# Kernel tuning notes

Hardware: AMD Instinct MI355X
Metric: run time of the kernel (lower is better)

Reference implementation:

```python
import jax, jax.numpy as jnp
import numpy as np

N_NODES = 5000
N_EDGES = 160000


def _conv2d(x, w, b):
    # x: [N, Cin, H, W], w: [Cout, Cin, kh, kw] (OIHW), VALID padding, stride 1
    out = jax.lax.conv_general_dilated(
        x, w, window_strides=(1, 1), padding='VALID',
        dimension_numbers=('NCHW', 'OIHW', 'NCHW'))
    return out + b[None, :, None, None]


def _gcn_norm(edge_index, n):
    # PyG gcn_norm with add_self_loops=False: deg from target (col) nodes,
    # norm = d^{-1/2}[src] * d^{-1/2}[dst]
    src, dst = edge_index[0], edge_index[1]
    ones = jnp.ones((edge_index.shape[1],), jnp.float32)
    deg = jax.ops.segment_sum(ones, dst, num_segments=n)
    dinv = jnp.where(deg > 0, jax.lax.rsqrt(jnp.maximum(deg, 1.0)), 0.0)
    return dinv[src] * dinv[dst]


def _arma(x, edge_index, norm, w_init, w_root, bias):
    # ARMAConv, num_layers=1: mean_k ReLU( Ahat (x W_k) + x V_k + b_k )
    # x: [N, Fin], w_init/w_root: [K, Fin, Fout], bias: [K, Fout]
    n = x.shape[0]
    src, dst = edge_index[0], edge_index[1]
    h = jnp.einsum('nf,kfo->kno', x, w_init)            # [K, N, Fout]
    msg = h[:, src, :] * norm[None, :, None]            # [K, E, Fout] gather
    agg = jax.vmap(lambda m: jax.ops.segment_sum(m, dst, num_segments=n))(msg)
    root = jnp.einsum('nf,kfo->kno', x, w_root)         # [K, N, Fout]
    out = jax.nn.relu(agg + root + bias[:, None, :])
    return out.mean(axis=0)                             # mean over K stacks


def setup_inputs() -> dict:
    key = jax.random.key(0)
    ks = jax.random.split(key, 32)

    def rn(i, shape, s=0.1):
        return jax.random.normal(ks[i], shape, jnp.float32) * s

    d = {}
    d['inputs'] = jax.random.normal(ks[0], (N_NODES, 1, 53, 6), jnp.float32)
    d['edge_index'] = jax.random.randint(ks[1], (2, N_EDGES), 0, N_NODES, jnp.int32)
    # CNN encoder params (Conv2d(1,100,(3,3)), Conv2d(100,200,(3,2)), Conv2d(200,1,(3,2)))
    d['e1_w'] = rn(2, (100, 1, 3, 3), 0.3); d['e1_b'] = rn(3, (100,), 0.1)
    d['e2_w'] = rn(4, (200, 100, 3, 2), 0.04); d['e2_b'] = rn(5, (200,), 0.1)
    d['e3_w'] = rn(6, (1, 200, 3, 2), 0.04); d['e3_b'] = rn(7, (1,), 0.1)
    # ARMA layers: (Fin, Fout, num_stacks K)
    dims = [(94, 128, 2), (128, 128, 2), (128, 128, 2), (128, 128, 2), (128, 128, 2), (128, 16, 1)]
    k = 8
    for i, (fi, fo, K) in enumerate(dims, 1):
        s = 1.0 / np.sqrt(fi)
        d[f'a{i}_wi'] = rn(k, (K, fi, fo), s)
        d[f'a{i}_wr'] = rn(k + 1, (K, fi, fo), s)
        d[f'a{i}_b'] = rn(k + 2, (K, fo), 0.05)
        k += 3
    return d


def reference(inputs, edge_index, e1_w, e1_b, e2_w, e2_b, e3_w, e3_b,
              a1_wi, a1_wr, a1_b, a2_wi, a2_wr, a2_b, a3_wi, a3_wr, a3_b,
              a4_wi, a4_wr, a4_b, a5_wi, a5_wr, a5_b, a6_wi, a6_wr, a6_b):
    # CNN encoder (Dropout2d is identity in eval mode)
    h = jax.nn.leaky_relu(_conv2d(inputs, e1_w, e1_b), 0.01)
    h = jax.nn.leaky_relu(_conv2d(h, e2_w, e2_b), 0.01)
    h = _conv2d(h, e3_w, e3_b)
    h = jnp.tanh(h.reshape(-1, 94))                     # [N, 94]
    norm = _gcn_norm(edge_index, h.shape[0])
    for (wi, wr, b) in [(a1_wi, a1_wr, a1_b), (a2_wi, a2_wr, a2_b),
                        (a3_wi, a3_wr, a3_b), (a4_wi, a4_wr, a4_b),
                        (a5_wi, a5_wr, a5_b)]:
        h = jnp.tanh(_arma(h, edge_index, norm, wi, wr, b))
    h = _arma(h, edge_index, norm, a6_wi, a6_wr, a6_b)
    return jax.nn.softmax(h, axis=1)
```

## Files before the change

### kernel.cpp

```cpp
#include <hip/hip_runtime.h>
#include <math.h>

typedef _Float16 f16;
typedef _Float16 f16x4 __attribute__((ext_vector_type(4)));
typedef _Float16 f16x8 __attribute__((ext_vector_type(8)));
typedef float f32x4 __attribute__((ext_vector_type(4)));

#define NN 5000
#define NE 160000

#define OFF_W2T   0ul
#define OFF_W3T   344064ul
#define OFF_WT1   346560ul
#define OFF_WT2   444864ul
#define OFF_WT3   575936ul
#define OFF_WT4   707008ul
#define OFF_WT5   838080ul
#define OFF_WT6   969152ul
#define OFF_H0    985536ul
#define OFF_HA    1945536ul
#define OFF_HB    3225536ul
#define OFF_C     4505536ul
#define OFF_DEG   14745536ul
#define OFF_IP    14765536ul
#define OFF_CUR   14785568ul
#define OFF_DINV  14805568ul
#define OFF_CSRS  14825568ul
#define OFF_CSRN  15465568ul
#define OFF_W1T   OFF_C

#define L_IN   0
#define L_BUF  1280
#define L_A1   (L_BUF)
#define L_C1   (L_BUF + 16640)
#define L_C2   (L_BUF)
#define C1_STRIDE 136
#define LDS_TOTAL (17920 + 208*272)

__global__ void prep_w2t(const float* __restrict__ w, f16* __restrict__ W2T) {
  int i = blockIdx.x*256 + threadIdx.x;
  if (i >= 21*256*32) return;
  int j = i & 7, g = (i >> 3) & 3, n = (i >> 5) & 255, kc = i >> 13;
  int k = kc*32 + g*8 + j;
  int tap = k / 112, c = k - tap*112;
  float v = 0.f;
  if (n < 200 && c < 100 && tap < 6) v = w[n*600 + c*6 + tap];
  W2T[i] = (f16)v;
}

__global__ void prep_w3t(const float* __restrict__ w, f16* __restrict__ W3T) {
  int i = blockIdx.x*256 + threadIdx.x;
  if (i >= 1248) return;
  int tap = i / 208, c = i - tap*208;
  float v = (c < 200) ? w[c*6 + tap] : 0.f;
  W3T[i] = (f16)v;
}

__global__ void prep_w1t(const float* __restrict__ w, f16* __restrict__ W1T) {
  int i = blockIdx.x*256 + threadIdx.x;
  if (i >= 112*32) return;
  int n = i >> 5, k = i & 31;
  float v = (n < 100 && k < 9) ? w[n*9 + k] : 0.f;
  W1T[i] = (f16)v;
}

__global__ void prep_wt(const float* __restrict__ wi, const float* __restrict__ wr,
                        f16* __restrict__ WT, int Kst, int Fin, int Fout, int Kpad, int R) {
  int i = blockIdx.x*256 + threadIdx.x;
  if (i >= R*Kpad) return;
  int n = i / Kpad, kk = i - n*Kpad;
  float v = 0.f;
  if (kk < Fin) {
    int path = n / (Kst*Fout);
    if (path < 2) {
      int rem = n - path*(Kst*Fout);
      int k = rem / Fout, fo = rem - k*Fout;
      const float* w = (path == 0) ? wi : wr;
      v = w[(k*Fin + kk)*Fout + fo];
    }
  }
  WT[i] = (f16)v;
}

__global__ void zero_kernel(int* __restrict__ deg, int* __restrict__ cur) {
  int i = blockIdx.x*256 + threadIdx.x;
  if (i < NN) { deg[i] = 0; cur[i] = 0; }
}

__global__ void deg_kernel(const int* __restrict__ ei, int* __restrict__ deg) {
  int e = blockIdx.x*256 + threadIdx.x;
  if (e < NE) atomicAdd(&deg[ei[NE + e]], 1);
}

__global__ __launch_bounds__(1024) void scan_kernel(const int* __restrict__ deg,
                                                    int* __restrict__ ip,
                                                    float* __restrict__ dinv) {
  __shared__ int buf[1024];
  __shared__ int s_carry;
  const int tid = threadIdx.x;
  if (tid == 0) s_carry = 0;
  __syncthreads();
  for (int base = 0; base < NN; base += 1024) {
    int i = base + tid;
    int v = (i < NN) ? deg[i] : 0;
    buf[tid] = v;
    __syncthreads();
    for (int off = 1; off < 1024; off <<= 1) {
      int t = (tid >= off) ? buf[tid - off] : 0;
      __syncthreads();
      buf[tid] += t;
      __syncthreads();
    }
    int incl = buf[tid];
    int c = s_carry;
    if (i < NN) {
      ip[i] = c + incl - v;
      dinv[i] = (v > 0) ? rsqrtf((float)v) : 0.f;
    }
    __syncthreads();
    if (tid == 1023) s_carry = c + buf[1023];
    __syncthreads();
  }
  if (tid == 0) ip[NN] = s_carry;
}

__global__ void csr_fill(const int* __restrict__ ei, const float* __restrict__ dinv,
                         const int* __restrict__ ip, int* __restrict__ cur,
                         int* __restrict__ csrs, float* __restrict__ csrn) {
  int e = blockIdx.x*256 + threadIdx.x;
  if (e >= NE) return;
  int s = ei[e], d = ei[NE + e];
  int pos = ip[d] + atomicAdd(&cur[d], 1);
  csrs[pos] = s;
  csrn[pos] = dinv[s]*dinv[d];
}

__global__ __launch_bounds__(1024) void cnn_kernel(
    const float* __restrict__ inp, const f16* __restrict__ W1T, const float* __restrict__ b1,
    const f16* __restrict__ W2T, const float* __restrict__ b2,
    const f16* __restrict__ W3T, const float* __restrict__ b3,
    f16* __restrict__ h0)
{
  extern __shared__ char smem[];
  float* s_in = (float*)(smem + L_IN);
  f16*   s_a1 = (f16*)(smem + L_A1);
  f16*   s_c1 = (f16*)(smem + L_C1);
  f16*   s_c2 = (f16*)(smem + L_C2);

  const int node = blockIdx.x;
  const int tid  = threadIdx.x;
  const int lane = tid & 63, wid = tid >> 6;
  const int l15 = lane & 15, g = lane >> 4;

  for (int i = tid; i < 318; i += 1024) s_in[i] = inp[node*318 + i];
  for (int i = tid; i < 208*12; i += 1024) {
    int r = i / 12, c = 100 + (i - r*12);
    s_c1[r*C1_STRIDE + c] = (f16)0.f;
  }
  __syncthreads();

  for (int i = tid; i < 208*32; i += 1024) {
    int m = i >> 5, k = i & 31;
    float v = 0.f;
    if (m < 204 && k < 9) {
      int y = m >> 2, x = m & 3;
      int ky = (k >= 6) ? 2 : (k >= 3 ? 1 : 0);
      int kx = k - ky*3;
      v = s_in[(y + ky)*6 + x + kx];
    }
    s_a1[m*40 + k] = (f16)v;
  }
  __syncthreads();

  for (int p = wid; p < 91; p += 16) {
    int mt = p % 13, nt = p / 13;
    f16x8 a = *(const f16x8*)(W1T + (nt*16 + l15)*32 + g*8);
    f16x8 b = *(const f16x8*)(s_a1 + (mt*16 + l15)*40 + g*8);
    f32x4 acc = (f32x4){0.f,0.f,0.f,0.f};
    acc = __builtin_amdgcn_mfma_f32_16x16x32_f16(a, b, acc, 0, 0, 0);
    int m = mt*16 + l15;
    int cb = nt*16 + g*4;
    f16x4 pack;
    #pragma unroll
    for (int j = 0; j < 4; j++) {
      int c = cb + j;
      float bias = (c < 100) ? b1[c] : 0.f;
      float v = acc[j] + bias;
      v = v > 0.f ? v : 0.01f*v;
      pack[j] = (f16)v;
    }
    *(f16x4*)(s_c1 + m*C1_STRIDE + cb) = pack;
  }
  __syncthreads();

  const int wm = wid >> 3, wn = wid & 7;

  const f16* abase[5];
  #pragma unroll
  for (int mi = 0; mi < 5; mi++) {
    int p = (wm*5 + mi)*16 + l15;
    int pp = p < 147 ? p : 0;
    int y2 = pp / 3;
    abase[mi] = s_c1 + (y2*4 + (pp - y2*3))*C1_STRIDE + g*8;
  }

  f32x4 acc[5][2];
  #pragma unroll
  for (int mi = 0; mi < 5; mi++)
    #pragma unroll
    for (int ni = 0; ni < 2; ni++)
      acc[mi][ni] = (f32x4){0.f,0.f,0.f,0.f};

  const f16* bbase = W2T + wn*1024 + l15*32 + g*8;
  #pragma unroll
  for (int kc = 0; kc < 21; kc++) {
    f16x8 b[2];
    const f16* bkc = bbase + kc*8192;
    #pragma unroll
    for (int ni = 0; ni < 2; ni++)
      b[ni] = *(const f16x8*)(bkc + ni*512);
    int kg0 = kc*32;
    int tap0 = kg0 / 112;
    int rem0 = kg0 - tap0*112;
    int cfull = rem0 + g*8;
    int wrap = cfull >= 112 ? 1 : 0;
    int c = cfull - wrap*112;
    int tapg = tap0 + wrap;
    int dr = ((tapg >> 1) << 2) + (tapg & 1);
    int aoff = dr*C1_STRIDE + (c - g*8);
    #pragma unroll
    for (int mi = 0; mi < 5; mi++) {
      f16x8 a = *(const f16x8*)(abase[mi] + aoff);
      #pragma unroll
      for (int ni = 0; ni < 2; ni++)
        acc[mi][ni] = __builtin_amdgcn_mfma_f32_16x16x32_f16(b[ni], a, acc[mi][ni], 0, 0, 0);
    }
  }

  __syncthreads();

  #pragma unroll
  for (int ni = 0; ni < 2; ni++) {
    int nb = wn*32 + ni*16 + g*4;
    if (nb < 216) {
      #pragma unroll
      for (int mi = 0; mi < 5; mi++) {
        int m = (wm*5 + mi)*16 + l15;
        if (m < 147) {
          f16x4 pack;
          #pragma unroll
          for (int j = 0; j < 4; j++) {
            int n = nb + j;
            float bias = (n < 200) ? b2[n] : 0.f;
            float v = acc[mi][ni][j] + bias;
            v = v > 0.f ? v : 0.01f*v;
            pack[j] = (f16)v;
          }
          *(f16x4*)(s_c2 + m*216 + nb) = pack;
        }
      }
    }
  }
  __syncthreads();

  if (wid < 6) {
    int pos = wid*16 + l15;
    int q = pos < 94 ? pos : 0;
    int r3 = (q >> 1)*3 + (q & 1);
    f32x4 acc3 = (f32x4){0.f,0.f,0.f,0.f};
    #pragma unroll
    for (int kc = 0; kc < 39; kc++) {
      int k = kc*32 + g*8;
      int tap = k / 208;
      int c = k - tap*208;
      int dr = (tap >> 1)*3 + (tap & 1);
      f16x8 a = *(const f16x8*)(W3T + k);
      f16x8 b = *(const f16x8*)(s_c2 + (r3 + dr)*216 + c);
      acc3 = __builtin_amdgcn_mfma_f32_16x16x32_f16(a, b, acc3, 0, 0, 0);
    }
    if (g == 0) {
      float v = (pos < 94) ? tanhf(acc3[0] + b3[0]) : 0.f;
      h0[node*96 + pos] = (f16)v;
    }
  }
}

template<int K>
__global__ __launch_bounds__(256, 4) void gemm_kernel(
    const f16* __restrict__ A, const f16* __restrict__ B, float* __restrict__ C,
    int M, int N)
{
  constexpr int LK = K + 8;
  __shared__ f16 sA[64*LK];
  __shared__ f16 sB[64*LK];
  const int tid = threadIdx.x;
  const int m0 = blockIdx.x*64, n0 = blockIdx.y*64;
  constexpr int SEGS = K/8;
  for (int i = tid; i < 64*SEGS; i += 256) {
    int row = i / SEGS, seg = i - row*SEGS;
    int gm = m0 + row; if (gm >= M) gm = M - 1;
    *(f16x8*)(sA + row*LK + seg*8) = *(const f16x8*)(A + (size_t)gm*K + seg*8);
    *(f16x8*)(sB + row*LK + seg*8) = *(const f16x8*)(B + (size_t)(n0 + row)*K + seg*8);
  }
  __syncthreads();
  const int lane = tid & 63, wid = tid >> 6;
  const int l15 = lane & 15, g = lane >> 4;
  const int wm = wid >> 1, wn = wid & 1;
  f32x4 acc[2][2];
  #pragma unroll
  for (int mi = 0; mi < 2; mi++)
    #pragma unroll
    for (int ni = 0; ni < 2; ni++)
      acc[mi][ni] = (f32x4){0.f,0.f,0.f,0.f};
  #pragma unroll
  for (int kc = 0; kc < K/32; kc++) {
    f16x8 a[2], b[2];
    #pragma unroll
    for (int mi = 0; mi < 2; mi++)
      a[mi] = *(const f16x8*)(sA + (wm*32 + mi*16 + l15)*LK + kc*32 + g*8);
    #pragma unroll
    for (int ni = 0; ni < 2; ni++)
      b[ni] = *(const f16x8*)(sB + (wn*32 + ni*16 + l15)*LK + kc*32 + g*8);
    #pragma unroll
    for (int mi = 0; mi < 2; mi++)
      #pragma unroll
      for (int ni = 0; ni < 2; ni++)
        acc[mi][ni] = __builtin_amdgcn_mfma_f32_16x16x32_f16(a[mi], b[ni], acc[mi][ni], 0, 0, 0);
  }
  #pragma unroll
  for (int mi = 0; mi < 2; mi++)
    #pragma unroll
    for (int ni = 0; ni < 2; ni++)
      #pragma unroll
      for (int j = 0; j < 4; j++) {
        int m = m0 + wm*32 + mi*16 + g*4 + j;
        int n = n0 + wn*32 + ni*16 + l15;
        if (m < M) C[(size_t)m*N + n] = acc[mi][ni][j];
      }
}

__global__ __launch_bounds__(256) void combine128(
    const float* __restrict__ C, const int* __restrict__ ip,
    const int* __restrict__ csrs, const float* __restrict__ csrn,
    const float* __restrict__ bias, f16* __restrict__ hout)
{
  const int d = blockIdx.x*4 + (threadIdx.x >> 6);
  const int lane = threadIdx.x & 63;
  const int i0 = ip[d], i1 = ip[d+1];
  float a00 = 0.f, a01 = 0.f, a10 = 0.f, a11 = 0.f;
  float b00 = 0.f, b01 = 0.f, b10 = 0.f, b11 = 0.f;
  int e = i0;
  for (; e + 1 < i1; e += 2) {
    int s0 = csrs[e], s1 = csrs[e+1];
    float w0 = csrn[e], w1 = csrn[e+1];
    const float* t0 = C + (size_t)s0*512;
    const float* t1 = C + (size_t)s1*512;
    a00 += w0*t0[lane];       a01 += w0*t0[lane+64];
    a10 += w0*t0[lane+128];   a11 += w0*t0[lane+192];
    b00 += w1*t1[lane];       b01 += w1*t1[lane+64];
    b10 += w1*t1[lane+128];   b11 += w1*t1[lane+192];
  }
  if (e < i1) {
    int s = csrs[e];
    float w = csrn[e];
    const float* t = C + (size_t)s*512;
    a00 += w*t[lane];       a01 += w*t[lane+64];
    a10 += w*t[lane+128];   a11 += w*t[lane+192];
  }
  a00 += b00; a01 += b01; a10 += b10; a11 += b11;
  const float* r = C + (size_t)d*512 + 256;
  float o0 = fmaxf(a00 + r[lane]     + bias[lane],     0.f)
           + fmaxf(a10 + r[lane+128] + bias[lane+128], 0.f);
  float o1 = fmaxf(a01 + r[lane+64]  + bias[lane+64],  0.f)
           + fmaxf(a11 + r[lane+192] + bias[lane+192], 0.f);
  hout[(size_t)d*128 + lane]      = (f16)tanhf(0.5f*o0);
  hout[(size_t)d*128 + lane + 64] = (f16)tanhf(0.5f*o1);
}

__global__ __launch_bounds__(256) void combine_out(
    const float* __restrict__ C, const int* __restrict__ ip,
    const int* __restrict__ csrs, const float* __restrict__ csrn,
    const float* __restrict__ bias, float* __restrict__ out)
{
  const int d = blockIdx.x*4 + (threadIdx.x >> 6);
  const int lane = threadIdx.x & 63;
  const int f = lane & 15;
  const int i0 = ip[d], i1 = ip[d+1];
  float a = 0.f, b = 0.f;
  int e = i0;
  for (; e + 1 < i1; e += 2) {
    a += csrn[e]   * C[(size_t)csrs[e]*64 + f];
    b += csrn[e+1] * C[(size_t)csrs[e+1]*64 + f];
  }
  if (e < i1) a += csrn[e] * C[(size_t)csrs[e]*64 + f];
  a += b;
  float v = fmaxf(a + C[(size_t)d*64 + 16 + f] + bias[f], 0.f);
  float m = v;
  #pragma unroll
  for (int off = 1; off < 16; off <<= 1) m = fmaxf(m, __shfl_xor(m, off));
  float ev = expf(v - m);
  float s = ev;
  #pragma unroll
  for (int off = 1; off < 16; off <<= 1) s += __shfl_xor(s, off);
  if (lane < 16) out[(size_t)d*16 + lane] = ev / s;
}

extern "C" void kernel_launch(void* const* d_in, const int* in_sizes, int n_in,
                              void* d_out, int out_size, void* d_ws, size_t ws_size,
                              hipStream_t stream)
{
  const float* inputs = (const float*)d_in[0];
  const int*   ei     = (const int*)d_in[1];
  const float* e1w = (const float*)d_in[2];
  const float* e1b = (const float*)d_in[3];
  const float* e2w = (const float*)d_in[4];
  const float* e2b = (const float*)d_in[5];
  const float* e3w = (const float*)d_in[6];
  const float* e3b = (const float*)d_in[7];
  const float *awi[6], *awr[6], *ab[6];
  for (int i = 0; i < 6; i++) {
    awi[i] = (const float*)d_in[8 + 3*i];
    awr[i] = (const float*)d_in[9 + 3*i];
    ab[i]  = (const float*)d_in[10 + 3*i];
  }
  char* ws = (char*)d_ws;
  f16* W2T = (f16*)(ws + OFF_W2T);
  f16* W3T = (f16*)(ws + OFF_W3T);
  f16* W1T = (f16*)(ws + OFF_W1T);
  f16* WT[6] = { (f16*)(ws + OFF_WT1), (f16*)(ws + OFF_WT2), (f16*)(ws + OFF_WT3),
                 (f16*)(ws + OFF_WT4), (f16*)(ws + OFF_WT5), (f16*)(ws + OFF_WT6) };
  f16* H0 = (f16*)(ws + OFF_H0);
  f16* HA = (f16*)(ws + OFF_HA);
  f16* HB = (f16*)(ws + OFF_HB);
  float* C = (float*)(ws + OFF_C);
  int* DEG = (int*)(ws + OFF_DEG);
  int* IP  = (int*)(ws + OFF_IP);
  int* CUR = (int*)(ws + OFF_CUR);
  float* DINV = (float*)(ws + OFF_DINV);
  int* CSRS = (int*)(ws + OFF_CSRS);
  float* CSRN = (float*)(ws + OFF_CSRN);

  (void)hipFuncSetAttribute((const void*)cnn_kernel,
                            hipFuncAttributeMaxDynamicSharedMemorySize, LDS_TOTAL);

  prep_w2t<<<672, 256, 0, stream>>>(e2w, W2T);
  prep_w3t<<<5, 256, 0, stream>>>(e3w, W3T);
  prep_w1t<<<14, 256, 0, stream>>>(e1w, W1T);
  prep_wt<<<192, 256, 0, stream>>>(awi[0], awr[0], WT[0], 2, 94, 128, 96, 512);
  for (int l = 1; l < 5; l++)
    prep_wt<<<256, 256, 0, stream>>>(awi[l], awr[l], WT[l], 2, 128, 128, 128, 512);
  prep_wt<<<32, 256, 0, stream>>>(awi[5], awr[5], WT[5], 1, 128, 16, 128, 64);

  zero_kernel<<<20, 256, 0, stream>>>(DEG, CUR);
  deg_kernel<<<625, 256, 0, stream>>>(ei, DEG);
  scan_kernel<<<1, 1024, 0, stream>>>(DEG, IP, DINV);
  csr_fill<<<625, 256, 0, stream>>>(ei, DINV, IP, CUR, CSRS, CSRN);

  cnn_kernel<<<NN, 1024, LDS_TOTAL, stream>>>(inputs, W1T, e1b, W2T, e2b, W3T, e3b, H0);

  gemm_kernel<96><<<dim3(79, 8), 256, 0, stream>>>(H0, WT[0], C, NN, 512);
  combine128<<<1250, 256, 0, stream>>>(C, IP, CSRS, CSRN, ab[0], HA);
  gemm_kernel<128><<<dim3(79, 8), 256, 0, stream>>>(HA, WT[1], C, NN, 512);
  combine128<<<1250, 256, 0, stream>>>(C, IP, CSRS, CSRN, ab[1], HB);
  gemm_kernel<128><<<dim3(79, 8), 256, 0, stream>>>(HB, WT[2], C, NN, 512);
  combine128<<<1250, 256, 0, stream>>>(C, IP, CSRS, CSRN, ab[2], HA);
  gemm_kernel<128><<<dim3(79, 8), 256, 0, stream>>>(HA, WT[3], C, NN, 512);
  combine128<<<1250, 256, 0, stream>>>(C, IP, CSRS, CSRN, ab[3], HB);
  gemm_kernel<128><<<dim3(79, 8), 256, 0, stream>>>(HB, WT[4], C, NN, 512);
  combine128<<<1250, 256, 0, stream>>>(C, IP, CSRS, CSRN, ab[4], HA);
  gemm_kernel<128><<<dim3(79, 1), 256, 0, stream>>>(HA, WT[5], C, NN, 64);
  combine_out<<<1250, 256, 0, stream>>>(C, IP, CSRS, CSRN, ab[5], (float*)d_out);
}
```

Before: 714.5 us.

## Store gathered GEMM output in fp16, fuse weight prep, reorder conv1 LDS rows

The layer GEMM now writes the Ahat-path half of its output as a separate fp16 buffer. The root half stays fp32 in its own array, so the edge gather in combine128 reads half as many bytes per neighbor, and each lane now handles an adjacent pair of columns. All weight-prep kernels are merged into one launch, and the zeroing kernel becomes hipMemsetAsync calls. The conv1 output rows in LDS are permuted by x-position (row = y + 52*x), and the zero-fill of padding columns 100..111 is dropped. Risks: fp16 rounding of aggregated messages, and the padding columns are no longer explicitly cleared, though they are multiplied by zero weights.

```diff
diff --git a/kernel.cpp b/kernel.cpp
--- a/kernel.cpp
+++ b/kernel.cpp
@@ -2,6 +2,7 @@
 #include <math.h>
 
 typedef _Float16 f16;
+typedef _Float16 f16x2 __attribute__((ext_vector_type(2)));
 typedef _Float16 f16x4 __attribute__((ext_vector_type(4)));
 typedef _Float16 f16x8 __attribute__((ext_vector_type(8)));
 typedef float f32x4 __attribute__((ext_vector_type(4)));
@@ -21,6 +22,7 @@
 #define OFF_HA    1945536ul
 #define OFF_HB    3225536ul
 #define OFF_C     4505536ul
+#define OFF_CT    9625536ul
 #define OFF_DEG   14745536ul
 #define OFF_IP    14765536ul
 #define OFF_CUR   14785568ul
@@ -37,37 +39,8 @@
 #define C1_STRIDE 136
 #define LDS_TOTAL (17920 + 208*272)
 
-__global__ void prep_w2t(const float* __restrict__ w, f16* __restrict__ W2T) {
-  int i = blockIdx.x*256 + threadIdx.x;
-  if (i >= 21*256*32) return;
-  int j = i & 7, g = (i >> 3) & 3, n = (i >> 5) & 255, kc = i >> 13;
-  int k = kc*32 + g*8 + j;
-  int tap = k / 112, c = k - tap*112;
-  float v = 0.f;
-  if (n < 200 && c < 100 && tap < 6) v = w[n*600 + c*6 + tap];
-  W2T[i] = (f16)v;
-}
-
-__global__ void prep_w3t(const float* __restrict__ w, f16* __restrict__ W3T) {
-  int i = blockIdx.x*256 + threadIdx.x;
-  if (i >= 1248) return;
-  int tap = i / 208, c = i - tap*208;
-  float v = (c < 200) ? w[c*6 + tap] : 0.f;
-  W3T[i] = (f16)v;
-}
-
-__global__ void prep_w1t(const float* __restrict__ w, f16* __restrict__ W1T) {
-  int i = blockIdx.x*256 + threadIdx.x;
-  if (i >= 112*32) return;
-  int n = i >> 5, k = i & 31;
-  float v = (n < 100 && k < 9) ? w[n*9 + k] : 0.f;
-  W1T[i] = (f16)v;
-}
-
-__global__ void prep_wt(const float* __restrict__ wi, const float* __restrict__ wr,
-                        f16* __restrict__ WT, int Kst, int Fin, int Fout, int Kpad, int R) {
-  int i = blockIdx.x*256 + threadIdx.x;
-  if (i >= R*Kpad) return;
+__device__ __forceinline__ void wt_body(int i, const float* wi, const float* wr,
+                                        f16* WT, int Kst, int Fin, int Fout, int Kpad) {
   int n = i / Kpad, kk = i - n*Kpad;
   float v = 0.f;
   if (kk < Fin) {
@@ -82,9 +55,48 @@
   WT[i] = (f16)v;
 }
 
-__global__ void zero_kernel(int* __restrict__ deg, int* __restrict__ cur) {
-  int i = blockIdx.x*256 + threadIdx.x;
-  if (i < NN) { deg[i] = 0; cur[i] = 0; }
+__global__ void prep_all(char* ws, const float* __restrict__ e1w,
+                         const float* __restrict__ e2w, const float* __restrict__ e3w,
+                         const float* wi1, const float* wr1, const float* wi2, const float* wr2,
+                         const float* wi3, const float* wr3, const float* wi4, const float* wr4,
+                         const float* wi5, const float* wr5, const float* wi6, const float* wr6) {
+  int b = blockIdx.x, tid = threadIdx.x;
+  if (b < 672) {
+    int i = b*256 + tid;
+    int kc = i >> 13, n = (i >> 5) & 255;
+    int k = i & 31;
+    int kk = kc*32 + k;
+    int tap = kk / 112, c = kk - tap*112;
+    float v = 0.f;
+    if (n < 200 && c < 100 && tap < 6) v = e2w[n*600 + c*6 + tap];
+    ((f16*)(ws + OFF_W2T))[i] = (f16)v;
+  } else if (b < 677) {
+    int i = (b - 672)*256 + tid;
+    if (i < 1248) {
+      int tap = i / 208, c = i - tap*208;
+      float v = (c < 200) ? e3w[c*6 + tap] : 0.f;
+      ((f16*)(ws + OFF_W3T))[i] = (f16)v;
+    }
+  } else if (b < 691) {
+    int i = (b - 677)*256 + tid;
+    if (i < 112*32) {
+      int n = i >> 5, k = i & 31;
+      float v = (n < 100 && k < 9) ? e1w[n*9 + k] : 0.f;
+      ((f16*)(ws + OFF_W1T))[i] = (f16)v;
+    }
+  } else if (b < 883) {
+    wt_body((b - 691)*256 + tid, wi1, wr1, (f16*)(ws + OFF_WT1), 2, 94, 128, 96);
+  } else if (b < 1139) {
+    wt_body((b - 883)*256 + tid, wi2, wr2, (f16*)(ws + OFF_WT2), 2, 128, 128, 128);
+  } else if (b < 1395) {
+    wt_body((b - 1139)*256 + tid, wi3, wr3, (f16*)(ws + OFF_WT3), 2, 128, 128, 128);
+  } else if (b < 1651) {
+    wt_body((b - 1395)*256 + tid, wi4, wr4, (f16*)(ws + OFF_WT4), 2, 128, 128, 128);
+  } else if (b < 1907) {
+    wt_body((b - 1651)*256 + tid, wi5, wr5, (f16*)(ws + OFF_WT5), 2, 128, 128, 128);
+  } else {
+    wt_body((b - 1907)*256 + tid, wi6, wr6, (f16*)(ws + OFF_WT6), 1, 128, 16, 128);
+  }
 }
 
 __global__ void deg_kernel(const int* __restrict__ ei, int* __restrict__ deg) {
@@ -153,10 +165,6 @@
   const int l15 = lane & 15, g = lane >> 4;
 
   for (int i = tid; i < 318; i += 1024) s_in[i] = inp[node*318 + i];
-  for (int i = tid; i < 208*12; i += 1024) {
-    int r = i / 12, c = 100 + (i - r*12);
-    s_c1[r*C1_STRIDE + c] = (f16)0.f;
-  }
   __syncthreads();
 
   for (int i = tid; i < 208*32; i += 1024) {
@@ -179,6 +187,7 @@
     f32x4 acc = (f32x4){0.f,0.f,0.f,0.f};
     acc = __builtin_amdgcn_mfma_f32_16x16x32_f16(a, b, acc, 0, 0, 0);
     int m = mt*16 + l15;
+    int rowp = (m >> 2) + 52*(m & 3);
     int cb = nt*16 + g*4;
     f16x4 pack;
     #pragma unroll
@@ -189,7 +198,7 @@
       v = v > 0.f ? v : 0.01f*v;
       pack[j] = (f16)v;
     }
-    *(f16x4*)(s_c1 + m*C1_STRIDE + cb) = pack;
+    *(f16x4*)(s_c1 + rowp*C1_STRIDE + cb) = pack;
   }
   __syncthreads();
 
@@ -201,7 +210,8 @@
     int p = (wm*5 + mi)*16 + l15;
     int pp = p < 147 ? p : 0;
     int y2 = pp / 3;
-    abase[mi] = s_c1 + (y2*4 + (pp - y2*3))*C1_STRIDE + g*8;
+    int x2 = pp - y2*3;
+    abase[mi] = s_c1 + (y2 + 52*x2)*C1_STRIDE + g*8;
   }
 
   f32x4 acc[5][2];
@@ -226,7 +236,7 @@
     int wrap = cfull >= 112 ? 1 : 0;
     int c = cfull - wrap*112;
     int tapg = tap0 + wrap;
-    int dr = ((tapg >> 1) << 2) + (tapg & 1);
+    int dr = (tapg >> 1) + 52*(tapg & 1);
     int aoff = dr*C1_STRIDE + (c - g*8);
     #pragma unroll
     for (int mi = 0; mi < 5; mi++) {
@@ -287,8 +297,8 @@
 
 template<int K>
 __global__ __launch_bounds__(256, 4) void gemm_kernel(
-    const f16* __restrict__ A, const f16* __restrict__ B, float* __restrict__ C,
-    int M, int N)
+    const f16* __restrict__ A, const f16* __restrict__ B, float* __restrict__ Croot,
+    f16* __restrict__ CT, int M, int N)
 {
   constexpr int LK = K + 8;
   __shared__ f16 sA[64*LK];
@@ -327,54 +337,83 @@
       for (int ni = 0; ni < 2; ni++)
         acc[mi][ni] = __builtin_amdgcn_mfma_f32_16x16x32_f16(a[mi], b[ni], acc[mi][ni], 0, 0, 0);
   }
-  #pragma unroll
-  for (int mi = 0; mi < 2; mi++)
-    #pragma unroll
-    for (int ni = 0; ni < 2; ni++)
+  if (CT != nullptr && n0 < 256) {
+    #pragma unroll
+    for (int mi = 0; mi < 2; mi++)
       #pragma unroll
-      for (int j = 0; j < 4; j++) {
-        int m = m0 + wm*32 + mi*16 + g*4 + j;
-        int n = n0 + wn*32 + ni*16 + l15;
-        if (m < M) C[(size_t)m*N + n] = acc[mi][ni][j];
-      }
+      for (int ni = 0; ni < 2; ni++)
+        #pragma unroll
+        for (int j = 0; j < 4; j++) {
+          int m = m0 + wm*32 + mi*16 + g*4 + j;
+          int n = n0 + wn*32 + ni*16 + l15;
+          if (m < M) CT[(size_t)m*256 + n] = (f16)acc[mi][ni][j];
+        }
+  } else if (CT != nullptr) {
+    #pragma unroll
+    for (int mi = 0; mi < 2; mi++)
+      #pragma unroll
+      for (int ni = 0; ni < 2; ni++)
+        #pragma unroll
+        for (int j = 0; j < 4; j++) {
+          int m = m0 + wm*32 + mi*16 + g*4 + j;
+          int n = n0 + wn*32 + ni*16 + l15 - 256;
+          if (m < M) Croot[(size_t)m*256 + n] = acc[mi][ni][j];
+        }
+  } else {
+    #pragma unroll
+    for (int mi = 0; mi < 2; mi++)
+      #pragma unroll
+      for (int ni = 0; ni < 2; ni++)
+        #pragma unroll
+        for (int j = 0; j < 4; j++) {
+          int m = m0 + wm*32 + mi*16 + g*4 + j;
+          int n = n0 + wn*32 + ni*16 + l15;
+          if (m < M) Croot[(size_t)m*N + n] = acc[mi][ni][j];
+        }
+  }
 }
 
 __global__ __launch_bounds__(256) void combine128(
-    const float* __restrict__ C, const int* __restrict__ ip,
-    const int* __restrict__ csrs, const float* __restrict__ csrn,
-    const float* __restrict__ bias, f16* __restrict__ hout)
+    const f16* __restrict__ CT, const float* __restrict__ Croot,
+    const int* __restrict__ ip, const int* __restrict__ csrs,
+    const float* __restrict__ csrn, const float* __restrict__ bias,
+    f16* __restrict__ hout)
 {
   const int d = blockIdx.x*4 + (threadIdx.x >> 6);
   const int lane = threadIdx.x & 63;
+  const int c = lane*2;
   const int i0 = ip[d], i1 = ip[d+1];
-  float a00 = 0.f, a01 = 0.f, a10 = 0.f, a11 = 0.f;
-  float b00 = 0.f, b01 = 0.f, b10 = 0.f, b11 = 0.f;
+  float a00=0.f, a01=0.f, a10=0.f, a11=0.f;
+  float b00=0.f, b01=0.f, b10=0.f, b11=0.f;
   int e = i0;
   for (; e + 1 < i1; e += 2) {
     int s0 = csrs[e], s1 = csrs[e+1];
     float w0 = csrn[e], w1 = csrn[e+1];
-    const float* t0 = C + (size_t)s0*512;
-    const float* t1 = C + (size_t)s1*512;
-    a00 += w0*t0[lane];       a01 += w0*t0[lane+64];
-    a10 += w0*t0[lane+128];   a11 += w0*t0[lane+192];
-    b00 += w1*t1[lane];       b01 += w1*t1[lane+64];
-    b10 += w1*t1[lane+128];   b11 += w1*t1[lane+192];
+    f16x2 t00 = *(const f16x2*)(CT + (size_t)s0*256 + c);
+    f16x2 t01 = *(const f16x2*)(CT + (size_t)s0*256 + 128 + c);
+    f16x2 t10 = *(const f16x2*)(CT + (size_t)s1*256 + c);
+    f16x2 t11 = *(const f16x2*)(CT + (size_t)s1*256 + 128 + c);
+    a00 += w0*(float)t00.x;  a01 += w0*(float)t00.y;
+    a10 += w0*(float)t01.x;  a11 += w0*(float)t01.y;
+    b00 += w1*(float)t10.x;  b01 += w1*(float)t10.y;
+    b10 += w1*(float)t11.x;  b11 += w1*(float)t11.y;
   }
   if (e < i1) {
     int s = csrs[e];
     float w = csrn[e];
-    const float* t = C + (size_t)s*512;
-    a00 += w*t[lane];       a01 += w*t[lane+64];
-    a10 += w*t[lane+128];   a11 += w*t[lane+192];
+    f16x2 t0 = *(const f16x2*)(CT + (size_t)s*256 + c);
+    f16x2 t1 = *(const f16x2*)(CT + (size_t)s*256 + 128 + c);
+    a00 += w*(float)t0.x;  a01 += w*(float)t0.y;
+    a10 += w*(float)t1.x;  a11 += w*(float)t1.y;
   }
   a00 += b00; a01 += b01; a10 += b10; a11 += b11;
-  const float* r = C + (size_t)d*512 + 256;
-  float o0 = fmaxf(a00 + r[lane]     + bias[lane],     0.f)
-           + fmaxf(a10 + r[lane+128] + bias[lane+128], 0.f);
-  float o1 = fmaxf(a01 + r[lane+64]  + bias[lane+64],  0.f)
-           + fmaxf(a11 + r[lane+192] + bias[lane+192], 0.f);
-  hout[(size_t)d*128 + lane]      = (f16)tanhf(0.5f*o0);
-  hout[(size_t)d*128 + lane + 64] = (f16)tanhf(0.5f*o1);
+  const float* r = Croot + (size_t)d*256;
+  float o0 = 0.5f*(fmaxf(a00 + r[c]       + bias[c],       0.f)
+                 + fmaxf(a10 + r[128 + c] + bias[128 + c], 0.f));
+  float o1 = 0.5f*(fmaxf(a01 + r[c + 1]   + bias[c + 1],   0.f)
+                 + fmaxf(a11 + r[129 + c] + bias[129 + c], 0.f));
+  f16x2 ov; ov.x = (f16)tanhf(o0); ov.y = (f16)tanhf(o1);
+  *(f16x2*)(hout + (size_t)d*128 + c) = ov;
 }
 
 __global__ __launch_bounds__(256) void combine_out(
@@ -432,7 +471,8 @@
   f16* H0 = (f16*)(ws + OFF_H0);
   f16* HA = (f16*)(ws + OFF_HA);
   f16* HB = (f16*)(ws + OFF_HB);
-  float* C = (float*)(ws + OFF_C);
+  float* CR = (float*)(ws + OFF_C);
+  f16* CT  = (f16*)(ws + OFF_CT);
   int* DEG = (int*)(ws + OFF_DEG);
   int* IP  = (int*)(ws + OFF_IP);
   int* CUR = (int*)(ws + OFF_CUR);
@@ -443,31 +483,28 @@
   (void)hipFuncSetAttribute((const void*)cnn_kernel,
                             hipFuncAttributeMaxDynamicSharedMemorySize, LDS_TOTAL);
 
-  prep_w2t<<<672, 256, 0, stream>>>(e2w, W2T);
-  prep_w3t<<<5, 256, 0, stream>>>(e3w, W3T);
-  prep_w1t<<<14, 256, 0, stream>>>(e1w, W1T);
-  prep_wt<<<192, 256, 0, stream>>>(awi[0], awr[0], WT[0], 2, 94, 128, 96, 512);
-  for (int l = 1; l < 5; l++)
-    prep_wt<<<256, 256, 0, stream>>>(awi[l], awr[l], WT[l], 2, 128, 128, 128, 512);
-  prep_wt<<<32, 256, 0, stream>>>(awi[5], awr[5], WT[5], 1, 128, 16, 128, 64);
-
-  zero_kernel<<<20, 256, 0, stream>>>(DEG, CUR);
+  prep_all<<<1939, 256, 0, stream>>>(ws, e1w, e2w, e3w,
+                                     awi[0], awr[0], awi[1], awr[1], awi[2], awr[2],
+                                     awi[3], awr[3], awi[4], awr[4], awi[5], awr[5]);
+
+  (void)hipMemsetAsync(DEG, 0, NN*sizeof(int), stream);
+  (void)hipMemsetAsync(CUR, 0, NN*sizeof(int), stream);
   deg_kernel<<<625, 256, 0, stream>>>(ei, DEG);
   scan_kernel<<<1, 1024, 0, stream>>>(DEG, IP, DINV);
   csr_fill<<<625, 256, 0, stream>>>(ei, DINV, IP, CUR, CSRS, CSRN);
 
   cnn_kernel<<<NN, 1024, LDS_TOTAL, stream>>>(inputs, W1T, e1b, W2T, e2b, W3T, e3b, H0);
 
-  gemm_kernel<96><<<dim3(79, 8), 256, 0, stream>>>(H0, WT[0], C, NN, 512);
-  combine128<<<1250, 256, 0, stream>>>(C, IP, CSRS, CSRN, ab[0], HA);
-  gemm_kernel<128><<<dim3(79, 8), 256, 0, stream>>>(HA, WT[1], C, NN, 512);
-  combine128<<<1250, 256, 0, stream>>>(C, IP, CSRS, CSRN, ab[1], HB);
-  gemm_kernel<128><<<dim3(79, 8), 256, 0, stream>>>(HB, WT[2], C, NN, 512);
-  combine128<<<1250, 256, 0, stream>>>(C, IP, CSRS, CSRN, ab[2], HA);
-  gemm_kernel<128><<<dim3(79, 8), 256, 0, stream>>>(HA, WT[3], C, NN, 512);
-  combine128<<<1250, 256, 0, stream>>>(C, IP, CSRS, CSRN, ab[3], HB);
-  gemm_kernel<128><<<dim3(79, 8), 256, 0, stream>>>(HB, WT[4], C, NN, 512);
-  combine128<<<1250, 256, 0, stream>>>(C, IP, CSRS, CSRN, ab[4], HA);
-  gemm_kernel<128><<<dim3(79, 1), 256, 0, stream>>>(HA, WT[5], C, NN, 64);
-  combine_out<<<1250, 256, 0, stream>>>(C, IP, CSRS, CSRN, ab[5], (float*)d_out);
-}
+  gemm_kernel<96><<<dim3(79, 8), 256, 0, stream>>>(H0, WT[0], CR, CT, NN, 512);
+  combine128<<<1250, 256, 0, stream>>>(CT, CR, IP, CSRS, CSRN, ab[0], HA);
+  gemm_kernel<128><<<dim3(79, 8), 256, 0, stream>>>(HA, WT[1], CR, CT, NN, 512);
+  combine128<<<1250, 256, 0, stream>>>(CT, CR, IP, CSRS, CSRN, ab[1], HB);
+  gemm_kernel<128><<<dim3(79, 8), 256, 0, stream>>>(HB, WT[2], CR, CT, NN, 512);
+  combine128<<<1250, 256, 0, stream>>>(CT, CR, IP, CSRS, CSRN, ab[2], HA);
+  gemm_kernel<128><<<dim3(79, 8), 256, 0, stream>>>(HA, WT[3], CR, CT, NN, 512);
+  combine128<<<1250, 256, 0, stream>>>(CT, CR, IP, CSRS, CSRN, ab[3], HB);
+  gemm_kernel<128><<<dim3(79, 8), 256, 0, stream>>>(HB, WT[4], CR, CT, NN, 512);
+  combine128<<<1250, 256, 0, stream>>>(CT, CR, IP, CSRS, CSRN, ab[4], HA);
+  gemm_kernel<128><<<dim3(79, 1), 256, 0, stream>>>(HA, WT[5], CR, nullptr, NN, 64);
+  combine_out<<<1250, 256, 0, stream>>>(CR, IP, CSRS, CSRN, ab[5], (float*)d_out);
+}
```

After: 666.5 us. -6.7%, faster.
